# Optimization experiments

Hardware: AMD Instinct MI355X
Metric: run time of the kernel (lower is better)

The kernel has to match this reference:

```python
import jax, jax.numpy as jnp
import numpy as np

N_AGENT = 25
N_S = 32
N_A = 4
HID = 128
EHH_HID = HID * N_AGENT          # 3200
INTER = 150                      # INTERMEDIATE_NODES
BATCH = 2048
N_EDGE = 300


def _leaky(x):
    return jnp.where(x >= 0, x, 0.01 * x)


def setup_inputs() -> dict:
    key = jax.random.key(0)
    ks = jax.random.split(key, 12)
    states = jax.random.normal(ks[0], (N_AGENT, BATCH, N_S), dtype=jnp.float32)
    ehh_w = jax.random.normal(ks[1], (N_AGENT * N_S, EHH_HID), dtype=jnp.float32) * 0.05
    anova = jax.random.normal(ks[2], (EHH_HID + INTER, N_AGENT), dtype=jnp.float32)
    w1 = jax.random.normal(ks[3], (N_AGENT, EHH_HID, 12), dtype=jnp.float32) * 0.02
    b1 = jax.random.normal(ks[4], (N_AGENT, 12), dtype=jnp.float32) * 0.02
    w2 = jax.random.normal(ks[5], (N_AGENT, 12, 12), dtype=jnp.float32) * 0.3
    b2 = jax.random.normal(ks[6], (N_AGENT, 12), dtype=jnp.float32) * 0.02
    w3 = jax.random.normal(ks[7], (N_AGENT, 12, N_A), dtype=jnp.float32) * 0.3
    b3 = jax.random.normal(ks[8], (N_AGENT, N_A), dtype=jnp.float32) * 0.02
    actions = jax.random.randint(ks[9], (N_AGENT, BATCH), 0, N_A, dtype=jnp.int32)
    # adjacency rows: (bi_att_row, neighbor_row_a, unused, neighbor_row_b)
    c0 = jax.random.randint(ks[10], (N_EDGE, 1), 0, INTER, dtype=jnp.int32)
    c13 = jax.random.randint(ks[11], (N_EDGE, 2), 0, EHH_HID, dtype=jnp.int32)
    adj = jnp.concatenate([c0, c13[:, :1], jnp.zeros((N_EDGE, 1), jnp.int32), c13[:, 1:]], axis=1)
    return {"states": states, "ehh_w": ehh_w, "anova": anova,
            "w1": w1, "b1": b1, "w2": w2, "b2": b2, "w3": w3, "b3": b3,
            "actions": actions, "adj": adj}


def reference(states, ehh_w, anova, w1, b1, w2, b2, w3, b3, actions, adj):
    # states: (A, B, S) -> ehh_s: (B, A*S)   (torch.cat(states, dim=1))
    B = states.shape[1]
    ehh_s = jnp.transpose(states, (1, 0, 2)).reshape(B, -1)
    # EHH normalization (BatchNorm, affine=False, batch stats) + linear + LeakyReLU
    mu = jnp.mean(ehh_s, axis=0, keepdims=True)
    var = jnp.var(ehh_s, axis=0, keepdims=True)
    ehh_n = (ehh_s - mu) * jax.lax.rsqrt(var + 1e-5)
    ehh_embedding = _leaky(ehh_n @ ehh_w)                    # (B, EHH_HID)

    # ANOVA attention assembly via adjacency scatter
    self_att = anova[:EHH_HID, :]                            # (EHH_HID, A)
    bi_att = anova[EHH_HID:, :]                              # (INTER, A)
    vals = bi_att[adj[:, 0], :]                              # (E, A)
    neighbor_att = jnp.zeros((EHH_HID, N_AGENT), jnp.float32)
    neighbor_att = neighbor_att.at[adj[:, 1]].set(vals)
    neighbor_att = neighbor_att.at[adj[:, 3]].set(vals)
    all_att = (self_att + neighbor_att).T                    # (A, EHH_HID)

    # att_s repeat/permute/reshape == broadcast of embedding per agent
    att_out = ehh_embedding[:, None, :] * all_att[None, :, :]  # (B, A, EHH_HID)

    # per-agent critics (ehh_hidden -> 12 -> 12 -> n_a)
    h1 = _leaky(jnp.einsum('bah,ahk->bak', att_out, w1) + b1[None])
    h2 = _leaky(jnp.einsum('bak,akj->baj', h1, w2) + b2[None])
    all_q = jnp.einsum('baj,ajc->bac', h2, w3) + b3[None]     # (B, A, N_A)

    # q = all_q.gather(1, in_acs) per agent -> (A, B)
    q = jnp.take_along_axis(all_q, actions.T[:, :, None], axis=2)[..., 0].T
    return q
```

## Files before the change

### kernel.cpp

```cpp
#include <hip/hip_runtime.h>
#include <cstdint>

#define NAG 25
#define NS 32
#define EHH 3200
#define KDIM 800
#define BATCH 2048
#define NEDGE 300
#define NPAD 384
#define KSPLIT 5

typedef _Float16 half8 __attribute__((ext_vector_type(8)));
typedef float f32x4 __attribute__((ext_vector_type(4)));

__device__ __forceinline__ float leaky(float x) { return x >= 0.f ? x : 0.01f * x; }

__global__ __launch_bounds__(256)
void prep1_kernel(const float* __restrict__ states, const float* __restrict__ ehh_w,
                  const int* __restrict__ adj, const float* __restrict__ anova,
                  const float* __restrict__ w1,
                  float* __restrict__ mean, float* __restrict__ rstd,
                  _Float16* __restrict__ wt, _Float16* __restrict__ w2dt) {
    __shared__ float redS[32][32];
    __shared__ float redQ[32][32];
    __shared__ float tile[32][33];
    __shared__ int win[EHH];
    const int bi = blockIdx.x;
    const int tid = threadIdx.x;

    if (bi < 25) {
        const int a = bi;
        const int s4 = (tid & 7) << 2;
        const int r0 = tid >> 3;
        const float* base = states + ((size_t)a * BATCH + r0) * NS + s4;
        f32x4 sum = {0.f, 0.f, 0.f, 0.f};
        f32x4 sq  = {0.f, 0.f, 0.f, 0.f};
#pragma unroll 8
        for (int it = 0; it < 64; ++it) {
            f32x4 v = *(const f32x4*)(base + (size_t)it * 32 * NS);
            sum += v;
            sq  += v * v;
        }
        *(f32x4*)&redS[r0][s4] = sum;
        *(f32x4*)&redQ[r0][s4] = sq;
        __syncthreads();
        if (tid < 32) {
            float s = 0.f, q = 0.f;
#pragma unroll
            for (int r = 0; r < 32; ++r) { s += redS[r][tid]; q += redQ[r][tid]; }
            float m = s * (1.f / BATCH);
            float var = q * (1.f / BATCH) - m * m;
            mean[a * 32 + tid] = m;
            rstd[a * 32 + tid] = rsqrtf(var + 1e-5f);
        }
    } else if (bi < 2525) {
        const int bb = bi - 25;
        const int n0 = (bb % 100) * 32, k0 = (bb / 100) * 32;
        const int x = tid & 31, y = tid >> 5;
        for (int i = y; i < 32; i += 8)
            tile[i][x] = ehh_w[(size_t)(k0 + i) * EHH + n0 + x];
        __syncthreads();
        for (int i = y; i < 32; i += 8)
            wt[(size_t)(n0 + i) * KDIM + k0 + x] = (_Float16)tile[x][i];
    } else {
        const int bb = bi - 2525;
        if (bb < 313) {
            for (int h = tid; h < EHH; h += 256) win[h] = -1;
            __syncthreads();
            for (int e = tid; e < 2 * NEDGE; e += 256) {
                int pass = e >= NEDGE;
                int ee = pass ? e - NEDGE : e;
                int dest = adj[ee * 4 + (pass ? 3 : 1)];
                atomicMax(&win[dest], e);
            }
            __syncthreads();
            int t = bb * 256 + tid;
            if (t < NAG * EHH) {
                int a = t / EHH;
                int h = t - a * EHH;
                float att = anova[(size_t)h * NAG + a];
                int w = win[h];
                if (w >= 0) {
                    int ee = w >= NEDGE ? w - NEDGE : w;
                    att += anova[(size_t)(EHH + adj[ee * 4]) * NAG + a];
                }
                const float* wp = w1 + ((size_t)a * EHH + h) * 12;
#pragma unroll
                for (int kk = 0; kk < 12; ++kk)
                    w2dt[(size_t)(a * 12 + kk) * EHH + h] = (_Float16)(att * wp[kk]);
            }
        } else {
            int p = (bb - 313) * 256 + tid;
            if (p < (NPAD - 300) * EHH / 8) {
                half8 z = {0, 0, 0, 0, 0, 0, 0, 0};
                ((half8*)(w2dt + (size_t)300 * EHH))[p] = z;
            }
        }
    }
}

__global__ __launch_bounds__(256)
void norm_kernel(const float* __restrict__ states, const float* __restrict__ mean,
                 const float* __restrict__ rstd, _Float16* __restrict__ A) {
    int u = blockIdx.x * 256 + threadIdx.x;
    int b = u / 100;
    int fo = (u - b * 100) * 8;
    int a = fo >> 5, s = fo & 31;
    const float* sp = states + ((size_t)a * BATCH + b) * NS + s;
    f32x4 v0 = *(const f32x4*)sp;
    f32x4 v1 = *(const f32x4*)(sp + 4);
    f32x4 m0 = *(const f32x4*)(mean + fo);
    f32x4 m1 = *(const f32x4*)(mean + fo + 4);
    f32x4 r0 = *(const f32x4*)(rstd + fo);
    f32x4 r1 = *(const f32x4*)(rstd + fo + 4);
    half8 out;
#pragma unroll
    for (int i = 0; i < 4; ++i) out[i] = (_Float16)((v0[i] - m0[i]) * r0[i]);
#pragma unroll
    for (int i = 0; i < 4; ++i) out[4 + i] = (_Float16)((v1[i] - m1[i]) * r1[i]);
    *(half8*)(A + (size_t)b * KDIM + fo) = out;
}

__device__ __forceinline__ void async16(const void* g, void* l) {
    __builtin_amdgcn_global_load_lds(
        (const __attribute__((address_space(1))) void*)(uintptr_t)g,
        (__attribute__((address_space(3))) void*)(unsigned)(uintptr_t)l, 16, 0, 0);
}

template <bool LEAKY_F16_OUT>
__global__ __launch_bounds__(256)
void gemm_bt(const _Float16* __restrict__ A, const _Float16* __restrict__ B,
             _Float16* __restrict__ Ch, float* __restrict__ Cf,
             int Ktot, int ldc, int kPerSplit, int slabStride) {
    __shared__ __attribute__((aligned(16))) _Float16 As[2][128 * 32];
    __shared__ __attribute__((aligned(16))) _Float16 Bs[2][128 * 32];
    const int tid = threadIdx.x;
    const int lane = tid & 63;
    const int wave = tid >> 6;
    const int wm = (wave >> 1) << 6;
    const int wn = (wave & 1) << 6;
    const int m0 = blockIdx.x << 7;
    const int n0 = blockIdx.y << 7;
    const int k0 = blockIdx.z * kPerSplit;
    const int nk = kPerSplit >> 5;

    const int srow = lane >> 2;
    const int scol = (lane & 3) << 3;
    const _Float16* gA0 = A + (size_t)(m0 + wave * 16 + srow) * Ktot + k0 + scol;
    const _Float16* gA1 = gA0 + (size_t)64 * Ktot;
    const _Float16* gB0 = B + (size_t)(n0 + wave * 16 + srow) * Ktot + k0 + scol;
    const _Float16* gB1 = gB0 + (size_t)64 * Ktot;
    const int lofs = wave * 512;

    f32x4 acc[4][4];
    const f32x4 zero = {0.f, 0.f, 0.f, 0.f};
#pragma unroll
    for (int i = 0; i < 4; ++i)
#pragma unroll
        for (int j = 0; j < 4; ++j) acc[i][j] = zero;

    const int fr = lane & 15;
    const int q8 = (lane >> 4) << 3;

    async16(gA0, As[0] + lofs);
    async16(gA1, As[0] + 2048 + lofs);
    async16(gB0, Bs[0] + lofs);
    async16(gB1, Bs[0] + 2048 + lofs);

    for (int kt = 0; kt < nk; ++kt) {
        const int cur = kt & 1;
        __syncthreads();
        if (kt + 1 < nk) {
            const int ko = (kt + 1) << 5;
            const int nxt = cur ^ 1;
            async16(gA0 + ko, As[nxt] + lofs);
            async16(gA1 + ko, As[nxt] + 2048 + lofs);
            async16(gB0 + ko, Bs[nxt] + lofs);
            async16(gB1 + ko, Bs[nxt] + 2048 + lofs);
        }
        half8 av[4], bv[4];
#pragma unroll
        for (int i = 0; i < 4; ++i)
            av[i] = *(const half8*)(As[cur] + (wm + i * 16 + fr) * 32 + q8);
#pragma unroll
        for (int j = 0; j < 4; ++j)
            bv[j] = *(const half8*)(Bs[cur] + (wn + j * 16 + fr) * 32 + q8);
#pragma unroll
        for (int i = 0; i < 4; ++i)
#pragma unroll
            for (int j = 0; j < 4; ++j)
                acc[i][j] = __builtin_amdgcn_mfma_f32_16x16x32_f16(av[i], bv[j], acc[i][j], 0, 0, 0);
    }

    const int r0 = (lane >> 4) << 2;
    if (LEAKY_F16_OUT) {
#pragma unroll
        for (int i = 0; i < 4; ++i)
#pragma unroll
            for (int j = 0; j < 4; ++j)
#pragma unroll
                for (int r = 0; r < 4; ++r) {
                    int row = m0 + wm + i * 16 + r0 + r;
                    int col = n0 + wn + j * 16 + fr;
                    Ch[(size_t)row * ldc + col] = (_Float16)leaky(acc[i][j][r]);
                }
    } else {
        float* C = Cf + (size_t)blockIdx.z * slabStride;
#pragma unroll
        for (int i = 0; i < 4; ++i)
#pragma unroll
            for (int j = 0; j < 4; ++j)
#pragma unroll
                for (int r = 0; r < 4; ++r) {
                    int row = m0 + wm + i * 16 + r0 + r;
                    int col = n0 + wn + j * 16 + fr;
                    C[(size_t)row * ldc + col] = acc[i][j][r];
                }
    }
}

__global__ void tail_kernel(const float* __restrict__ Hp, const float* __restrict__ b1,
                            const float* __restrict__ w2, const float* __restrict__ b2,
                            const float* __restrict__ w3, const float* __restrict__ b3,
                            const int* __restrict__ act, float* __restrict__ out) {
    int t = blockIdx.x * 256 + threadIdx.x;
    int b = t & (BATCH - 1);
    int a = t >> 11;
    const float* hp = Hp + (size_t)b * NPAD + a * 12;
    float h1[12];
#pragma unroll
    for (int k = 0; k < 12; ++k) {
        float s = b1[a * 12 + k];
#pragma unroll
        for (int ks = 0; ks < KSPLIT; ++ks) s += hp[(size_t)ks * BATCH * NPAD + k];
        h1[k] = leaky(s);
    }
    float h2[12];
#pragma unroll
    for (int j = 0; j < 12; ++j) {
        float s = b2[a * 12 + j];
#pragma unroll
        for (int k = 0; k < 12; ++k) s += h1[k] * w2[(a * 12 + k) * 12 + j];
        h2[j] = leaky(s);
    }
    int c = act[t];
    float q = b3[a * 4 + c];
#pragma unroll
    for (int j = 0; j < 12; ++j) q += h2[j] * w3[(a * 12 + j) * 4 + c];
    out[t] = q;
}

extern "C" void kernel_launch(void* const* d_in, const int* in_sizes, int n_in,
                              void* d_out, int out_size, void* d_ws, size_t ws_size,
                              hipStream_t stream) {
    (void)in_sizes; (void)n_in; (void)out_size; (void)ws_size;
    const float* states = (const float*)d_in[0];
    const float* ehh_w  = (const float*)d_in[1];
    const float* anova  = (const float*)d_in[2];
    const float* w1     = (const float*)d_in[3];
    const float* b1     = (const float*)d_in[4];
    const float* w2     = (const float*)d_in[5];
    const float* b2     = (const float*)d_in[6];
    const float* w3     = (const float*)d_in[7];
    const float* b3     = (const float*)d_in[8];
    const int* actions  = (const int*)d_in[9];
    const int* adj      = (const int*)d_in[10];
    float* out = (float*)d_out;

    char* ws = (char*)d_ws;
    float*     mean   = (float*)    (ws + 0);
    float*     rstd   = (float*)    (ws + 4096);
    _Float16*  Abf    = (_Float16*) (ws + 32768);
    _Float16*  WbT    = (_Float16*) (ws + 3311616);
    _Float16*  W2dT   = (_Float16*) (ws + 8433664);
    _Float16*  emb    = (_Float16*) (ws + 10893312);
    float*     Hp     = (float*)    (ws + 24002560);

    prep1_kernel<<<2970, 256, 0, stream>>>(states, ehh_w, adj, anova, w1,
                                           mean, rstd, WbT, W2dT);
    norm_kernel<<<800, 256, 0, stream>>>(states, mean, rstd, Abf);
    gemm_bt<true><<<dim3(16, 25, 1), 256, 0, stream>>>(Abf, WbT, emb, nullptr, KDIM, EHH, KDIM, 0);
    gemm_bt<false><<<dim3(16, 3, KSPLIT), 256, 0, stream>>>(emb, W2dT, nullptr, Hp, EHH, NPAD,
                                                            EHH / KSPLIT, BATCH * NPAD);
    tail_kernel<<<(BATCH * NAG) / 256, 256, 0, stream>>>(Hp, b1, w2, b2, w3, b3, actions, out);
}
```

Before: 133.4 us.

## Fold batch-norm into GEMM weights and bias instead of normalizing activations

```diff
diff --git a/kernel.cpp b/kernel.cpp
--- a/kernel.cpp
+++ b/kernel.cpp
@@ -15,28 +15,30 @@
 
 __device__ __forceinline__ float leaky(float x) { return x >= 0.f ? x : 0.01f * x; }
 
+#define STATS_B 50
+#define CAST_B  800
+#define W2D_B   445
+#define ZERO_B  13
 __global__ __launch_bounds__(256)
-void prep1_kernel(const float* __restrict__ states, const float* __restrict__ ehh_w,
-                  const int* __restrict__ adj, const float* __restrict__ anova,
-                  const float* __restrict__ w1,
-                  float* __restrict__ mean, float* __restrict__ rstd,
-                  _Float16* __restrict__ wt, _Float16* __restrict__ w2dt) {
+void prep_kernel(const float* __restrict__ states, const float* __restrict__ w1,
+                 const float* __restrict__ anova, const int* __restrict__ adj,
+                 float* __restrict__ acc, float* __restrict__ cvec,
+                 _Float16* __restrict__ A, _Float16* __restrict__ w2dt) {
     __shared__ float redS[32][32];
     __shared__ float redQ[32][32];
-    __shared__ float tile[32][33];
     __shared__ int win[EHH];
     const int bi = blockIdx.x;
     const int tid = threadIdx.x;
 
-    if (bi < 25) {
-        const int a = bi;
+    if (bi < STATS_B) {
+        const int a = bi >> 1, hf = bi & 1;
         const int s4 = (tid & 7) << 2;
         const int r0 = tid >> 3;
-        const float* base = states + ((size_t)a * BATCH + r0) * NS + s4;
+        const float* base = states + ((size_t)a * BATCH + hf * 1024 + r0) * NS + s4;
         f32x4 sum = {0.f, 0.f, 0.f, 0.f};
         f32x4 sq  = {0.f, 0.f, 0.f, 0.f};
 #pragma unroll 8
-        for (int it = 0; it < 64; ++it) {
+        for (int it = 0; it < 32; ++it) {
             f32x4 v = *(const f32x4*)(base + (size_t)it * 32 * NS);
             sum += v;
             sq  += v * v;
@@ -48,22 +50,25 @@
             float s = 0.f, q = 0.f;
 #pragma unroll
             for (int r = 0; r < 32; ++r) { s += redS[r][tid]; q += redQ[r][tid]; }
-            float m = s * (1.f / BATCH);
-            float var = q * (1.f / BATCH) - m * m;
-            mean[a * 32 + tid] = m;
-            rstd[a * 32 + tid] = rsqrtf(var + 1e-5f);
+            acc[hf * 800 + a * 32 + tid] = s;
+            acc[1600 + hf * 800 + a * 32 + tid] = q;
         }
-    } else if (bi < 2525) {
-        const int bb = bi - 25;
-        const int n0 = (bb % 100) * 32, k0 = (bb / 100) * 32;
-        const int x = tid & 31, y = tid >> 5;
-        for (int i = y; i < 32; i += 8)
-            tile[i][x] = ehh_w[(size_t)(k0 + i) * EHH + n0 + x];
-        __syncthreads();
-        for (int i = y; i < 32; i += 8)
-            wt[(size_t)(n0 + i) * KDIM + k0 + x] = (_Float16)tile[x][i];
-    } else {
-        const int bb = bi - 2525;
+    } else if (bi < STATS_B + CAST_B) {
+        int u = (bi - STATS_B) * 256 + tid;
+        int b = u / 100;
+        int fo = (u - b * 100) * 8;
+        int a = fo >> 5, s = fo & 31;
+        const float* sp = states + ((size_t)a * BATCH + b) * NS + s;
+        f32x4 v0 = *(const f32x4*)sp;
+        f32x4 v1 = *(const f32x4*)(sp + 4);
+        half8 o;
+#pragma unroll
+        for (int i = 0; i < 4; ++i) o[i] = (_Float16)v0[i];
+#pragma unroll
+        for (int i = 0; i < 4; ++i) o[4 + i] = (_Float16)v1[i];
+        *(half8*)(A + (size_t)b * KDIM + fo) = o;
+    } else if (bi < STATS_B + CAST_B + W2D_B) {
+        const int bb = bi - (STATS_B + CAST_B);
         if (bb < 313) {
             for (int h = tid; h < EHH; h += 256) win[h] = -1;
             __syncthreads();
@@ -96,29 +101,50 @@
                 ((half8*)(w2dt + (size_t)300 * EHH))[p] = z;
             }
         }
+    } else {
+        int t = (bi - (STATS_B + CAST_B + W2D_B)) * 256 + tid;
+        if (t < EHH) cvec[t] = 0.f;
     }
 }
 
 __global__ __launch_bounds__(256)
-void norm_kernel(const float* __restrict__ states, const float* __restrict__ mean,
-                 const float* __restrict__ rstd, _Float16* __restrict__ A) {
-    int u = blockIdx.x * 256 + threadIdx.x;
-    int b = u / 100;
-    int fo = (u - b * 100) * 8;
-    int a = fo >> 5, s = fo & 31;
-    const float* sp = states + ((size_t)a * BATCH + b) * NS + s;
-    f32x4 v0 = *(const f32x4*)sp;
-    f32x4 v1 = *(const f32x4*)(sp + 4);
-    f32x4 m0 = *(const f32x4*)(mean + fo);
-    f32x4 m1 = *(const f32x4*)(mean + fo + 4);
-    f32x4 r0 = *(const f32x4*)(rstd + fo);
-    f32x4 r1 = *(const f32x4*)(rstd + fo + 4);
-    half8 out;
-#pragma unroll
-    for (int i = 0; i < 4; ++i) out[i] = (_Float16)((v0[i] - m0[i]) * r0[i]);
-#pragma unroll
-    for (int i = 0; i < 4; ++i) out[4 + i] = (_Float16)((v1[i] - m1[i]) * r1[i]);
-    *(half8*)(A + (size_t)b * KDIM + fo) = out;
+void wscale_kernel(const float* __restrict__ ehh_w, const float* __restrict__ acc,
+                   float* __restrict__ cvec, _Float16* __restrict__ wt) {
+    __shared__ float tile[32][129];
+    __shared__ float mL[32], rL[32];
+    __shared__ float cpart[2][128];
+    const int bk = blockIdx.x / 25, bn = blockIdx.x % 25;
+    const int k0 = bk * 32, n0 = bn * 128;
+    const int tid = threadIdx.x;
+    if (tid < 32) {
+        int f = k0 + tid;
+        float s = acc[f] + acc[800 + f];
+        float q = acc[1600 + f] + acc[2400 + f];
+        float m = s * (1.f / BATCH);
+        float var = q * (1.f / BATCH) - m * m;
+        mL[tid] = m;
+        rL[tid] = rsqrtf(var + 1e-5f);
+    }
+    __syncthreads();
+    const int x = tid & 127, y = tid >> 7;
+    float csum = 0.f;
+    for (int i = y; i < 32; i += 2) {
+        float v = ehh_w[(size_t)(k0 + i) * EHH + n0 + x] * rL[i];
+        tile[i][x] = v;
+        csum += mL[i] * v;
+    }
+    cpart[y][x] = csum;
+    __syncthreads();
+    if (tid < 128) atomicAdd(&cvec[n0 + tid], -(cpart[0][tid] + cpart[1][tid]));
+    const int n = tid & 127, h = tid >> 7;
+    half8 o0, o1;
+#pragma unroll
+    for (int j = 0; j < 8; ++j) o0[j] = (_Float16)tile[h * 16 + j][n];
+#pragma unroll
+    for (int j = 0; j < 8; ++j) o1[j] = (_Float16)tile[h * 16 + 8 + j][n];
+    _Float16* wp = wt + (size_t)(n0 + n) * KDIM + k0 + h * 16;
+    *(half8*)wp = o0;
+    *(half8*)(wp + 8) = o1;
 }
 
 __device__ __forceinline__ void async16(const void* g, void* l) {
@@ -131,6 +157,7 @@
 __global__ __launch_bounds__(256)
 void gemm_bt(const _Float16* __restrict__ A, const _Float16* __restrict__ B,
              _Float16* __restrict__ Ch, float* __restrict__ Cf,
+             const float* __restrict__ bias,
              int Ktot, int ldc, int kPerSplit, int slabStride) {
     __shared__ __attribute__((aligned(16))) _Float16 As[2][128 * 32];
     __shared__ __attribute__((aligned(16))) _Float16 Bs[2][128 * 32];
@@ -194,6 +221,9 @@
 
     const int r0 = (lane >> 4) << 2;
     if (LEAKY_F16_OUT) {
+        float cj[4];
+#pragma unroll
+        for (int j = 0; j < 4; ++j) cj[j] = bias[n0 + wn + j * 16 + fr];
 #pragma unroll
         for (int i = 0; i < 4; ++i)
 #pragma unroll
@@ -202,7 +232,7 @@
                 for (int r = 0; r < 4; ++r) {
                     int row = m0 + wm + i * 16 + r0 + r;
                     int col = n0 + wn + j * 16 + fr;
-                    Ch[(size_t)row * ldc + col] = (_Float16)leaky(acc[i][j][r]);
+                    Ch[(size_t)row * ldc + col] = (_Float16)leaky(acc[i][j][r] + cj[j]);
                 }
     } else {
         float* C = Cf + (size_t)blockIdx.z * slabStride;
@@ -268,19 +298,20 @@
     float* out = (float*)d_out;
 
     char* ws = (char*)d_ws;
-    float*     mean   = (float*)    (ws + 0);
-    float*     rstd   = (float*)    (ws + 4096);
+    float*     acc    = (float*)    (ws + 0);
+    float*     cvec   = (float*)    (ws + 16384);
     _Float16*  Abf    = (_Float16*) (ws + 32768);
     _Float16*  WbT    = (_Float16*) (ws + 3311616);
     _Float16*  W2dT   = (_Float16*) (ws + 8433664);
     _Float16*  emb    = (_Float16*) (ws + 10893312);
     float*     Hp     = (float*)    (ws + 24002560);
 
-    prep1_kernel<<<2970, 256, 0, stream>>>(states, ehh_w, adj, anova, w1,
-                                           mean, rstd, WbT, W2dT);
-    norm_kernel<<<800, 256, 0, stream>>>(states, mean, rstd, Abf);
-    gemm_bt<true><<<dim3(16, 25, 1), 256, 0, stream>>>(Abf, WbT, emb, nullptr, KDIM, EHH, KDIM, 0);
-    gemm_bt<false><<<dim3(16, 3, KSPLIT), 256, 0, stream>>>(emb, W2dT, nullptr, Hp, EHH, NPAD,
-                                                            EHH / KSPLIT, BATCH * NPAD);
+    prep_kernel<<<STATS_B + CAST_B + W2D_B + ZERO_B, 256, 0, stream>>>(
+        states, w1, anova, adj, acc, cvec, Abf, W2dT);
+    wscale_kernel<<<625, 256, 0, stream>>>(ehh_w, acc, cvec, WbT);
+    gemm_bt<true><<<dim3(16, 25, 1), 256, 0, stream>>>(Abf, WbT, emb, nullptr, cvec,
+                                                       KDIM, EHH, KDIM, 0);
+    gemm_bt<false><<<dim3(16, 3, KSPLIT), 256, 0, stream>>>(emb, W2dT, nullptr, Hp, nullptr,
+                                                            EHH, NPAD, EHH / KSPLIT, BATCH * NPAD);
     tail_kernel<<<(BATCH * NAG) / 256, 256, 0, stream>>>(Hp, b1, w2, b2, w3, b3, actions, out);
 }
```

Result: slower. 137.9 us (+3.4%).
